# Kernel tuning notes

Measured on AMD Instinct MI355X. Metric: run time of the kernel, lower is better.

Reference implementation:

```python
import jax, jax.numpy as jnp
import numpy as np

K = 21                     # kernel_size
LAM = 128.0                # lam
SIGMA_SPACE = 32.0
SIGMA_LUMA = 8.0
H = 512
W = 512
HO = H - K + 1             # valid conv output height (492)
WO = W - K + 1
C = (K - 1) // 2           # center offset (10)
CTR = C * K + C            # center channel index in row-major K*K patches


def _diff_patches(x):
    """x: (H, W) float. Returns (K*K-1, HO, WO): center pixel minus each
    of the other K*K-1 window taps (== the sparse 2-tap conv in torch)."""
    p = jax.lax.conv_general_dilated_patches(
        x[None, None], (K, K), (1, 1), 'VALID')[0]      # (K*K, HO, WO)
    diffs = p[CTR][None] - p                             # center - neighbor
    return jnp.delete(diffs, CTR, axis=0)                # drop all-zero center chan


def _make_w_ij(ref_hwc):
    """Bilateral affinity weights, per the torch __init__."""
    pos_x = jnp.broadcast_to(jnp.arange(W, dtype=jnp.float32)[None, :], (H, W))
    pos_y = jnp.broadcast_to(jnp.arange(H, dtype=jnp.float32)[:, None], (H, W))
    dx = _diff_patches(pos_x)
    dy = _diff_patches(pos_y)
    log_w = -(dx * dx + dy * dy) / (2.0 * SIGMA_SPACE ** 2)
    for c in range(ref_hwc.shape[-1]):                   # fixed 3 channels
        dr = _diff_patches(ref_hwc[:, :, c])
        log_w = log_w - dr * dr / (2.0 * SIGMA_LUMA ** 2)
    return jnp.exp(log_w)                                # (K*K-1, HO, WO)


def setup_inputs() -> dict:
    key = jax.random.key(0)
    k1, k2, k3 = jax.random.split(key, 3)
    output = jax.random.uniform(k1, (H, W), dtype=jnp.float32)   # logits/255
    target = jax.random.uniform(k2, (H, W), dtype=jnp.float32)   # target/255
    ref = jax.random.uniform(k3, (H, W, 3), dtype=jnp.float32) * 255.0
    w_ij = _make_w_ij(ref)
    bias = jnp.zeros((K * K - 1,), dtype=jnp.float32)   # torch conv bias (zeroed)
    return {"output": output, "target": target, "w_ij": w_ij, "bias": bias}


def reference(output, target, w_ij, bias):
    d = _diff_patches(output) + bias[:, None, None]      # (K*K-1, HO, WO)
    smooth = (H * W) * LAM * jnp.mean(w_ij * d * d)
    fidelity = jnp.mean((output - target) ** 2)
    return smooth + fidelity
```

## Files before the change

### kernel.cpp

```cpp
#include <hip/hip_runtime.h>

constexpr int Kk   = 21;
constexpr int Hh   = 512, Ww = 512;
constexpr int HO   = 492, WO = 492;
constexpr int Cc   = 10;
constexpr int CTRi = 220;
constexpr int NCH  = 440;
constexpr int ROW4 = WO / 4;
constexpr int N4F  = Hh * Ww / 4;

constexpr int RSPLIT = HO / 2;
constexpr int CSPLIT = 8;
constexpr int NPB    = NCH / CSPLIT;
constexpr int NBLK   = RSPLIT * CSPLIT;

constexpr float SCALE_S  = (float)((512.0 * 512.0 * 128.0) / (440.0 * 492.0 * 492.0));
constexpr float FID_RATIO = (float)((1.0 / (512.0 * 512.0)) /
                                    ((512.0 * 512.0 * 128.0) / (440.0 * 492.0 * 492.0)));

typedef float floatx4  __attribute__((ext_vector_type(4)));
typedef float floatx4u __attribute__((ext_vector_type(4), aligned(4)));

#define TPB 256

__device__ __forceinline__ float block_reduce_256(float v) {
    #pragma unroll
    for (int off = 32; off; off >>= 1) v += __shfl_down(v, off, 64);
    __shared__ float smem[TPB / 64];
    const int lane = threadIdx.x & 63;
    const int wid  = threadIdx.x >> 6;
    if (lane == 0) smem[wid] = v;
    __syncthreads();
    float r = 0.f;
    if (threadIdx.x == 0) {
        #pragma unroll
        for (int k = 0; k < TPB / 64; ++k) r += smem[k];
    }
    return r;
}

__global__ __launch_bounds__(TPB) void main_kernel(
        const float* __restrict__ outp,
        const float* __restrict__ targ,
        const float* __restrict__ w,
        const float* __restrict__ bias,
        float* __restrict__ partial)
{
    const int t = threadIdx.x;
    float acc = 0.f;

    {
        const int fq = blockIdx.x * TPB + t;
        if (fq < N4F) {
            const floatx4 a  = ((const floatx4*)outp)[fq];
            const floatx4 tg = ((const floatx4*)targ)[fq];
            const float d0 = a.x - tg.x, d1 = a.y - tg.y,
                        d2 = a.z - tg.z, d3 = a.w - tg.w;
            acc = (d0 * d0 + d1 * d1 + d2 * d2 + d3 * d3) * FID_RATIO;
        }
    }

    const int rowblk = blockIdx.x % RSPLIT;
    const int csplit = blockIdx.x / RSPLIT;
    const int n0     = csplit * NPB;

    if (t < 2 * ROW4) {
        const int di = (t >= ROW4) ? 1 : 0;
        const int j4 = t - di * ROW4;
        const int i  = rowblk * 2 + di;
        const int j  = 4 * j4;

        const float* crow = outp + (i + Cc) * Ww + (Cc + j);
        const float c0 = crow[0], c1 = crow[1], c2 = crow[2], c3 = crow[3];

        const float* obase = outp + i * Ww + j;
        const floatx4* wp  = (const floatx4*)w + ((long)(n0 * HO + i) * ROW4 + j4);

        float a0 = 0.f, a1 = 0.f, a2 = 0.f, a3 = 0.f;
        #pragma unroll 5
        for (int n = n0; n < n0 + NPB; ++n, wp += HO * ROW4) {
            const int kk = n + (n >= CTRi ? 1 : 0);
            const int ki = kk / Kk;
            const int kj = kk - ki * Kk;

            const floatx4  w4 = *wp;
            const float    b  = bias[n];
            const floatx4u n4 = *(const floatx4u*)(obase + ki * Ww + kj);

            const float d0 = c0 - n4.x + b;
            const float d1 = c1 - n4.y + b;
            const float d2 = c2 - n4.z + b;
            const float d3 = c3 - n4.w + b;

            a0 += w4.x * d0 * d0;
            a1 += w4.y * d1 * d1;
            a2 += w4.z * d2 * d2;
            a3 += w4.w * d3 * d3;
        }
        acc += (a0 + a1) + (a2 + a3);
    }

    const float bsum = block_reduce_256(acc);
    if (t == 0) partial[blockIdx.x] = bsum;
}

__global__ __launch_bounds__(TPB) void finalize_kernel(
        const float* __restrict__ partial,
        float* __restrict__ out)
{
    float v = 0.f;
    for (int idx = threadIdx.x; idx < NBLK; idx += TPB) v += partial[idx];
    const float s = block_reduce_256(v);
    if (threadIdx.x == 0) out[0] = s * SCALE_S;
}

extern "C" void kernel_launch(void* const* d_in, const int* in_sizes, int n_in,
                              void* d_out, int out_size, void* d_ws, size_t ws_size,
                              hipStream_t stream) {
    const float* outp = (const float*)d_in[0];
    const float* targ = (const float*)d_in[1];
    const float* w    = (const float*)d_in[2];
    const float* bias = (const float*)d_in[3];

    float* partial = (float*)d_ws;

    main_kernel<<<NBLK, TPB, 0, stream>>>(outp, targ, w, bias, partial);
    finalize_kernel<<<1, TPB, 0, stream>>>(partial, (float*)d_out);
}
```

Before: 549.4 us.

## Assign each block one channel plane chunk with contiguous nontemporal weight streaming

Reorganizes the work split so each block handles a contiguous chunk of rows within a single channel plane of the weight tensor, rather than a row pair across 55 channels. Weight reads become long contiguous streams per block and use nontemporal loads to avoid polluting cache. In exchange, the center pixels are reloaded per channel rather than kept in registers, and the grid grows to 2640 blocks, which adds more partial sums to reduce. The fidelity term still covers all pixels because the block count exceeds the number of float4 groups.

New measurement: 571.9 us. 1.04x slower.

```diff
diff --git a/kernel.cpp b/kernel.cpp
--- a/kernel.cpp
+++ b/kernel.cpp
@@ -9,10 +9,11 @@
 constexpr int ROW4 = WO / 4;
 constexpr int N4F  = Hh * Ww / 4;
 
-constexpr int RSPLIT = HO / 2;
-constexpr int CSPLIT = 8;
-constexpr int NPB    = NCH / CSPLIT;
-constexpr int NBLK   = RSPLIT * CSPLIT;
+constexpr int PLANE4 = HO * ROW4;
+constexpr int SPLITS = 6;
+constexpr int RPS    = HO / SPLITS;
+constexpr int CHUNK4 = RPS * ROW4;
+constexpr int NBLK   = NCH * SPLITS;
 
 constexpr float SCALE_S  = (float)((512.0 * 512.0 * 128.0) / (440.0 * 492.0 * 492.0));
 constexpr float FID_RATIO = (float)((1.0 / (512.0 * 512.0)) /
@@ -60,45 +61,37 @@
         }
     }
 
-    const int rowblk = blockIdx.x % RSPLIT;
-    const int csplit = blockIdx.x / RSPLIT;
-    const int n0     = csplit * NPB;
+    const int n  = blockIdx.x / SPLITS;
+    const int s  = blockIdx.x - n * SPLITS;
+    const int kk = n + (n >= CTRi ? 1 : 0);
+    const int ki = kk / Kk;
+    const int kj = kk - ki * Kk;
+    const float b = bias[n];
 
-    if (t < 2 * ROW4) {
-        const int di = (t >= ROW4) ? 1 : 0;
-        const int j4 = t - di * ROW4;
-        const int i  = rowblk * 2 + di;
-        const int j  = 4 * j4;
+    const floatx4* wplane = (const floatx4*)w + (long)n * PLANE4;
+    const int lo = s * CHUNK4;
+    const int hi = lo + CHUNK4;
 
-        const float* crow = outp + (i + Cc) * Ww + (Cc + j);
-        const float c0 = crow[0], c1 = crow[1], c2 = crow[2], c3 = crow[3];
+    float a0 = 0.f, a1 = 0.f, a2 = 0.f, a3 = 0.f;
+    for (int idx = lo + t; idx < hi; idx += TPB) {
+        const int r   = idx / ROW4;
+        const int col = (idx - r * ROW4) * 4;
 
-        const float* obase = outp + i * Ww + j;
-        const floatx4* wp  = (const floatx4*)w + ((long)(n0 * HO + i) * ROW4 + j4);
+        const floatx4  w4 = __builtin_nontemporal_load(wplane + idx);
+        const floatx4u c4 = *(const floatx4u*)(outp + (r + Cc) * Ww + (Cc + col));
+        const floatx4u n4 = *(const floatx4u*)(outp + (r + ki) * Ww + (kj + col));
 
-        float a0 = 0.f, a1 = 0.f, a2 = 0.f, a3 = 0.f;
-        #pragma unroll 5
-        for (int n = n0; n < n0 + NPB; ++n, wp += HO * ROW4) {
-            const int kk = n + (n >= CTRi ? 1 : 0);
-            const int ki = kk / Kk;
-            const int kj = kk - ki * Kk;
+        const float d0 = c4.x - n4.x + b;
+        const float d1 = c4.y - n4.y + b;
+        const float d2 = c4.z - n4.z + b;
+        const float d3 = c4.w - n4.w + b;
 
-            const floatx4  w4 = *wp;
-            const float    b  = bias[n];
-            const floatx4u n4 = *(const floatx4u*)(obase + ki * Ww + kj);
-
-            const float d0 = c0 - n4.x + b;
-            const float d1 = c1 - n4.y + b;
-            const float d2 = c2 - n4.z + b;
-            const float d3 = c3 - n4.w + b;
-
-            a0 += w4.x * d0 * d0;
-            a1 += w4.y * d1 * d1;
-            a2 += w4.z * d2 * d2;
-            a3 += w4.w * d3 * d3;
-        }
-        acc += (a0 + a1) + (a2 + a3);
+        a0 += w4.x * d0 * d0;
+        a1 += w4.y * d1 * d1;
+        a2 += w4.z * d2 * d2;
+        a3 += w4.w * d3 * d3;
     }
+    acc += (a0 + a1) + (a2 + a3);
 
     const float bsum = block_reduce_256(acc);
     if (t == 0) partial[blockIdx.x] = bsum;
```
